# Kernel optimization log

Measured on AMD Instinct MI355X. Metric: run time of the kernel, lower is better.

The kernel has to match this reference:

```python
import jax, jax.numpy as jnp
import numpy as np

N = 50000      # nodes
E = 800000     # edges (before self loops)
F_IN = 128     # num_features
H = 4          # heads
C = 32         # hidden_channels (per-head out dim)
L = 64         # num_labels


def gatv2_conv(x, src, dst, Wl, Wr, att, b, n):
    """PyG GATv2Conv (concat=True, negative_slope=0.2), self loops already in src/dst."""
    h, c = att.shape
    xl = (x @ Wl).reshape(n, h, c)          # source-side transform
    xr = (x @ Wr).reshape(n, h, c)          # target-side transform
    z = jax.nn.leaky_relu(xl[src] + xr[dst], 0.2)   # [Etot, H, C]
    e = jnp.einsum('ehc,hc->eh', z, att)            # attention logits per edge/head
    m = jax.ops.segment_max(e, dst, num_segments=n)  # per-destination softmax (stable)
    p = jnp.exp(e - m[dst])
    s = jax.ops.segment_sum(p, dst, num_segments=n)
    alpha = p / s[dst]                               # [Etot, H]
    out = jax.ops.segment_sum(xl[src] * alpha[..., None], dst, num_segments=n)
    return out.reshape(n, h * c) + b


def setup_inputs() -> dict:
    key = jax.random.key(0)
    ks = jax.random.split(key, 16)
    sc = 0.1
    return {
        'x': jax.random.normal(ks[0], (N, F_IN), dtype=jnp.float32),
        'edge_index': jax.random.randint(ks[1], (2, E), 0, N),
        # conv1: F_IN -> H*C
        'Wl1': jax.random.normal(ks[2], (F_IN, H * C), dtype=jnp.float32) * sc,
        'Wr1': jax.random.normal(ks[3], (F_IN, H * C), dtype=jnp.float32) * sc,
        'att1': jax.random.normal(ks[4], (H, C), dtype=jnp.float32) * sc,
        'b1': jnp.zeros((H * C,), dtype=jnp.float32),
        # conv2: H*C -> H*C
        'Wl2': jax.random.normal(ks[5], (H * C, H * C), dtype=jnp.float32) * sc,
        'Wr2': jax.random.normal(ks[6], (H * C, H * C), dtype=jnp.float32) * sc,
        'att2': jax.random.normal(ks[7], (H, C), dtype=jnp.float32) * sc,
        'b2': jnp.zeros((H * C,), dtype=jnp.float32),
        # MLP head
        'W1': jax.random.normal(ks[8], (H * C, L * 10), dtype=jnp.float32) * sc,
        'bb1': jnp.zeros((L * 10,), dtype=jnp.float32),
        'W2': jax.random.normal(ks[9], (L * 10, L * 5), dtype=jnp.float32) * sc,
        'bb2': jnp.zeros((L * 5,), dtype=jnp.float32),
        'W3': jax.random.normal(ks[10], (L * 5, L), dtype=jnp.float32) * sc,
        'bb3': jnp.zeros((L,), dtype=jnp.float32),
    }


def reference(x, edge_index, Wl1, Wr1, att1, b1, Wl2, Wr2, att2, b2,
              W1, bb1, W2, bb2, W3, bb3):
    loops = jnp.arange(N, dtype=edge_index.dtype)
    src = jnp.concatenate([edge_index[0], loops])
    dst = jnp.concatenate([edge_index[1], loops])
    h = jax.nn.elu(gatv2_conv(x, src, dst, Wl1, Wr1, att1, b1, N))
    h = jax.nn.elu(gatv2_conv(h, src, dst, Wl2, Wr2, att2, b2, N))
    h = jax.nn.elu(h @ W1 + bb1)
    h = jax.nn.elu(h @ W2 + bb2)
    return jax.nn.sigmoid(h @ W3 + bb3)
```

## Files before the change

### kernel.cpp

```cpp
#include <hip/hip_runtime.h>
#include <cstdint>
#include <cstddef>

typedef _Float16 f16;
typedef __attribute__((ext_vector_type(2))) _Float16 f16x2;
typedef __attribute__((ext_vector_type(4))) _Float16 f16x4;
typedef __attribute__((ext_vector_type(8))) _Float16 f16x8;
typedef __attribute__((ext_vector_type(4))) float f32x4;
typedef unsigned int u32;
typedef unsigned short u16;

#define ROWCAP 48
#define BCAP   5120
#define ECH    4096

__device__ __forceinline__ float fast_elu(float v)
{
    return v > 0.f ? v : __expf(v) - 1.f;
}
__device__ __forceinline__ float fast_sigmoid(float v)
{
    return 1.f / (1.f + __expf(-v));
}

__device__ __forceinline__ void gload16(const f16* g, f16* l)
{
    __builtin_amdgcn_global_load_lds(
        (const __attribute__((address_space(1))) u32*)g,
        (__attribute__((address_space(3))) u32*)l, 16, 0, 0);
}

#define BM 128
#define BN 64
#define BK 64

__global__ __launch_bounds__(256)
void gemm_mfma(const f16* __restrict__ A, const f16* __restrict__ Bt,
               const float* __restrict__ bias,
               float* __restrict__ Cf, f16* __restrict__ Cp,
               int M, int N, int K, int act)
{
    __shared__ __align__(16) f16 sA[BM * BK];
    __shared__ __align__(16) f16 sB[BN * BK];
    const int t = threadIdx.x;
    const int w = t >> 6, lane = t & 63;
    const int lr = lane & 15, lg = lane >> 4;

    const int nwg = gridDim.x * gridDim.y;
    int orig = blockIdx.y * gridDim.x + blockIdx.x;
    int q = nwg >> 3, r = nwg & 7;
    int xcd = orig & 7, slotid = orig >> 3;
    int wgid = (xcd < r ? xcd * (q + 1) : r * (q + 1) + (xcd - r) * q) + slotid;
    int bx = wgid % gridDim.x;
    int by = wgid / gridDim.x;

    const int row0 = by * BM, col0 = bx * BN;
    const int wr = (w & 1) * 64, wc = (w >> 1) * 32;
    const int srow = lane >> 3, slot = lane & 7;

    f32x4 acc[4][2];
    #pragma unroll
    for (int m = 0; m < 4; ++m)
        #pragma unroll
        for (int n = 0; n < 2; ++n) acc[m][n] = (f32x4)0.f;

    for (int k0 = 0; k0 < K; k0 += BK) {
        #pragma unroll
        for (int i = 0; i < 4; ++i) {
            int ci = w * 4 + i;
            int row = ci * 8 + srow;
            const f16* g = A + (size_t)(row0 + row) * K + k0 + ((slot ^ (row & 7)) << 3);
            gload16(g, &sA[ci * 512]);
        }
        #pragma unroll
        for (int i = 0; i < 2; ++i) {
            int ci = w * 2 + i;
            int col = ci * 8 + srow;
            const f16* g = Bt + (size_t)(col0 + col) * K + k0 + ((slot ^ (col & 7)) << 3);
            gload16(g, &sB[ci * 512]);
        }
        __syncthreads();
        #pragma unroll
        for (int kk = 0; kk < 2; ++kk) {
            f16x8 af[4], bfr[2];
            #pragma unroll
            for (int m = 0; m < 4; ++m) {
                int row = wr + m * 16 + lr;
                af[m] = *(const f16x8*)&sA[row * 64 + (((kk * 4 + lg) ^ (lr & 7)) << 3)];
            }
            #pragma unroll
            for (int n = 0; n < 2; ++n) {
                int col = wc + n * 16 + lr;
                bfr[n] = *(const f16x8*)&sB[col * 64 + (((kk * 4 + lg) ^ (lr & 7)) << 3)];
            }
            #pragma unroll
            for (int m = 0; m < 4; ++m)
                #pragma unroll
                for (int n = 0; n < 2; ++n)
                    acc[m][n] = __builtin_amdgcn_mfma_f32_16x16x32_f16(af[m], bfr[n], acc[m][n], 0, 0, 0);
        }
        __syncthreads();
    }

    #pragma unroll
    for (int m = 0; m < 4; ++m) {
        int grow = row0 + wr + m * 16 + lg * 4;
        #pragma unroll
        for (int n = 0; n < 2; ++n) {
            int gcol = col0 + wc + n * 16 + lr;
            if (gcol >= N) continue;
            float bv = bias ? bias[gcol] : 0.f;
            #pragma unroll
            for (int q2 = 0; q2 < 4; ++q2) {
                int rr = grow + q2;
                if (rr >= M) continue;
                float v = acc[m][n][q2] + bv;
                if (act == 1)      v = fast_elu(v);
                else if (act == 2) v = fast_sigmoid(v);
                size_t o = (size_t)rr * N + gcol;
                if (Cf) Cf[o] = v;
                else Cp[o] = (f16)v;
            }
        }
    }
}

__global__ __launch_bounds__(256)
void gemm_mfma_f32a(const float* __restrict__ A32, const f16* __restrict__ Bt,
                    f16* __restrict__ Cp, int M, int N, int K)
{
    __shared__ __align__(16) f16 sA[BM * BK];
    __shared__ __align__(16) f16 sB[BN * BK];
    const int t = threadIdx.x;
    const int w = t >> 6, lane = t & 63;
    const int lr = lane & 15, lg = lane >> 4;

    const int nwg = gridDim.x * gridDim.y;
    int orig = blockIdx.y * gridDim.x + blockIdx.x;
    int q = nwg >> 3, r = nwg & 7;
    int xcd = orig & 7, slotid = orig >> 3;
    int wgid = (xcd < r ? xcd * (q + 1) : r * (q + 1) + (xcd - r) * q) + slotid;
    int bx = wgid % gridDim.x;
    int by = wgid / gridDim.x;

    const int row0 = by * BM, col0 = bx * BN;
    const int wr = (w & 1) * 64, wc = (w >> 1) * 32;
    const int srow = lane >> 3, slot = lane & 7;

    f32x4 acc[4][2];
    #pragma unroll
    for (int m = 0; m < 4; ++m)
        #pragma unroll
        for (int n = 0; n < 2; ++n) acc[m][n] = (f32x4)0.f;

    for (int k0 = 0; k0 < K; k0 += BK) {
        #pragma unroll
        for (int i = 0; i < 4; ++i) {
            int ci = w * 4 + i;
            int row = ci * 8 + srow;
            int grow = row0 + row;
            const float* g = A32 + (size_t)grow * K + k0 + ((slot ^ (row & 7)) << 3);
            float4 v0 = make_float4(0.f, 0.f, 0.f, 0.f), v1 = v0;
            if (grow < M) {
                v0 = *(const float4*)g;
                v1 = *(const float4*)(g + 4);
            }
            f16x8 h;
            h[0] = (f16)v0.x; h[1] = (f16)v0.y; h[2] = (f16)v0.z; h[3] = (f16)v0.w;
            h[4] = (f16)v1.x; h[5] = (f16)v1.y; h[6] = (f16)v1.z; h[7] = (f16)v1.w;
            *(f16x8*)&sA[ci * 512 + (lane << 3)] = h;
        }
        #pragma unroll
        for (int i = 0; i < 2; ++i) {
            int ci = w * 2 + i;
            int col = ci * 8 + srow;
            const f16* g = Bt + (size_t)(col0 + col) * K + k0 + ((slot ^ (col & 7)) << 3);
            gload16(g, &sB[ci * 512]);
        }
        __syncthreads();
        #pragma unroll
        for (int kk = 0; kk < 2; ++kk) {
            f16x8 af[4], bfr[2];
            #pragma unroll
            for (int m = 0; m < 4; ++m) {
                int row = wr + m * 16 + lr;
                af[m] = *(const f16x8*)&sA[row * 64 + (((kk * 4 + lg) ^ (lr & 7)) << 3)];
            }
            #pragma unroll
            for (int n = 0; n < 2; ++n) {
                int col = wc + n * 16 + lr;
                bfr[n] = *(const f16x8*)&sB[col * 64 + (((kk * 4 + lg) ^ (lr & 7)) << 3)];
            }
            #pragma unroll
            for (int m = 0; m < 4; ++m)
                #pragma unroll
                for (int n = 0; n < 2; ++n)
                    acc[m][n] = __builtin_amdgcn_mfma_f32_16x16x32_f16(af[m], bfr[n], acc[m][n], 0, 0, 0);
        }
        __syncthreads();
    }

    #pragma unroll
    for (int m = 0; m < 4; ++m) {
        int grow = row0 + wr + m * 16 + lg * 4;
        #pragma unroll
        for (int n = 0; n < 2; ++n) {
            int gcol = col0 + wc + n * 16 + lr;
            if (gcol >= N) continue;
            #pragma unroll
            for (int q2 = 0; q2 < 4; ++q2) {
                int rr = grow + q2;
                if (rr >= M) continue;
                Cp[(size_t)rr * N + gcol] = (f16)acc[m][n][q2];
            }
        }
    }
}

__global__ __launch_bounds__(256)
void prep_kernel(const float* __restrict__ Wl1, const float* __restrict__ Wr1,
                 const float* __restrict__ Wl2, const float* __restrict__ Wr2,
                 f16* __restrict__ T1c, f16* __restrict__ T2c,
                 const float* __restrict__ W1, const float* __restrict__ W2,
                 const float* __restrict__ W3,
                 f16* __restrict__ T1, f16* __restrict__ T2, f16* __restrict__ T3,
                 const int* __restrict__ ei, int E, int Etot,
                 int* __restrict__ gcnt, u32* __restrict__ bucketbuf,
                 int nbwc, int nbwm)
{
    int b = blockIdx.x;
    int tid = threadIdx.x;
    if (b < nbwc) {
        int i = b * 256 + tid;
        int sel = i >> 15;
        int j = i & 32767;
        int r = j >> 7, k = j & 127, n = r & 127;
        const float* W = sel ? (r < 128 ? Wl2 : Wr2) : (r < 128 ? Wl1 : Wr1);
        f16* T = sel ? T2c : T1c;
        T[(size_t)r * 128 + k] = (f16)W[(size_t)k * 128 + n];
        return;
    }
    if (b < nbwc + nbwm) {
        int i = (b - nbwc) * 256 + tid;
        const int n1 = 640 * 128, n2 = 320 * 640, n3 = 64 * 320;
        if (i < n1) {
            int n = i >> 7, k = i & 127;
            T1[i] = (f16)W1[(size_t)k * 640 + n];
        } else if (i < n1 + n2) {
            int j = i - n1;
            int n = j / 640, k = j - n * 640;
            T2[j] = (f16)W2[(size_t)k * 320 + n];
        } else if (i < n1 + n2 + n3) {
            int j = i - n1 - n2;
            int n = j / 320, k = j - n * 320;
            T3[j] = (f16)W3[(size_t)k * 64 + n];
        }
        return;
    }
    __shared__ int hist[256];
    __shared__ int base[256];
    int bb = b - nbwc - nbwm;
    int e0 = bb * ECH;
    hist[tid] = 0;
    __syncthreads();

    u32 pk[ECH / 256];
    #pragma unroll
    for (int i = 0; i < ECH / 256; ++i) {
        int e = e0 + i * 256 + tid;
        u32 p = 0xFFFFFFFFu;
        if (e < Etot) {
            int src, dst;
            if (e < E) {
                src = __builtin_nontemporal_load(ei + e);
                dst = __builtin_nontemporal_load(ei + E + e);
            } else {
                src = dst = e - E;
            }
            p = ((u32)dst << 16) | (u32)src;
            atomicAdd(&hist[dst >> 8], 1);
        }
        pk[i] = p;
    }
    __syncthreads();
    int h = hist[tid];
    base[tid] = h ? atomicAdd(&gcnt[tid], h) : 0;
    __syncthreads();
    hist[tid] = 0;
    __syncthreads();
    #pragma unroll
    for (int i = 0; i < ECH / 256; ++i) {
        u32 p = pk[i];
        if (p != 0xFFFFFFFFu) {
            int bu = p >> 24;
            int pos = base[bu] + atomicAdd(&hist[bu], 1);
            if (pos < BCAP)
                bucketbuf[(size_t)bu * BCAP + pos] = p;
        }
    }
}

__global__ __launch_bounds__(256)
void bucket2_kernel(const int* __restrict__ gcnt, const u32* __restrict__ bucketbuf,
                    int* __restrict__ cnt, u16* __restrict__ csrcp, int N)
{
    __shared__ u16 rows[256 * ROWCAP];
    __shared__ int rc[256];
    const int bu = blockIdx.x;
    const int tid = threadIdx.x;
    rc[tid] = 0;
    __syncthreads();

    int total = gcnt[bu];
    if (total > BCAP) total = BCAP;
    const u32* bp = bucketbuf + (size_t)bu * BCAP;
    for (int i = tid; i < total; i += 256) {
        u32 p = bp[i];
        int nid = (p >> 16) & 255;
        int pos = atomicAdd(&rc[nid], 1);
        if (pos < ROWCAP) rows[nid * ROWCAP + pos] = (u16)(p & 0xFFFFu);
    }
    __syncthreads();

    const int node0 = bu * 256;
    u32* d = (u32*)(csrcp + (size_t)node0 * ROWCAP);
    const u32* s = (const u32*)rows;
    const int nwords = 256 * ROWCAP / 2;
    for (int j = tid; j < nwords; j += 256) d[j] = s[j];
    int node = node0 + tid;
    if (node < N) {
        int c = rc[tid];
        cnt[node] = c < ROWCAP ? c : ROWCAP;
    }
}

__device__ __forceinline__ float dot2acc(f16x2 a, f16x2 b, float c)
{
#if __has_builtin(__builtin_amdgcn_fdot2)
    return __builtin_amdgcn_fdot2(a, b, c, false);
#else
    return c + (float)a.x * (float)b.x + (float)a.y * (float)b.y;
#endif
}

__device__ __forceinline__ f16x2 lrelu2(f16x2 v, f16x2 c02)
{
    return __builtin_elementwise_max(v, v * c02);
}

__global__ __launch_bounds__(256)
void gat_fused(const f16* __restrict__ xlxr,
               const int* __restrict__ cnt, const u16* __restrict__ csrcp,
               const float* __restrict__ att, const float* __restrict__ bias,
               f16* __restrict__ outp, int N)
{
    const int tid  = threadIdx.x;
    const int wave = tid >> 6;
    const int lane = tid & 63;
    const int half = lane >> 5;
    const int hl   = lane & 31;
    const int node = blockIdx.x * 8 + wave * 2 + half;
    const int c    = hl * 4;

    const bool valid = node < N;
    const int nd = valid ? node : 0;

    f16x2 alo; alo.x = (f16)att[c];     alo.y = (f16)att[c + 1];
    f16x2 ahi; ahi.x = (f16)att[c + 2]; ahi.y = (f16)att[c + 3];
    f16x2 c02; c02.x = (f16)0.2f;       c02.y = (f16)0.2f;
    f16x4 xr4 = *(const f16x4*)(xlxr + (size_t)nd * 256 + 128 + c);
    f16x2 xrlo = __builtin_shufflevector(xr4, xr4, 0, 1);
    f16x2 xrhi = __builtin_shufflevector(xr4, xr4, 2, 3);

    float acc0 = 0.f, acc1 = 0.f, acc2 = 0.f, acc3 = 0.f, s = 0.f;
    int e   = valid ? nd * ROWCAP : 0;
    int end = valid ? e + cnt[nd] : 0;

    for (; e + 4 <= end; e += 4) {
        int s0 = csrcp[e], s1 = csrcp[e + 1], s2 = csrcp[e + 2], s3 = csrcp[e + 3];
        f16x4 xa = *(const f16x4*)(xlxr + (size_t)s0 * 256 + c);
        f16x4 xb = *(const f16x4*)(xlxr + (size_t)s1 * 256 + c);
        f16x4 xc = *(const f16x4*)(xlxr + (size_t)s2 * 256 + c);
        f16x4 xd = *(const f16x4*)(xlxr + (size_t)s3 * 256 + c);
        f16x2 xalo = __builtin_shufflevector(xa, xa, 0, 1);
        f16x2 xahi = __builtin_shufflevector(xa, xa, 2, 3);
        f16x2 xblo = __builtin_shufflevector(xb, xb, 0, 1);
        f16x2 xbhi = __builtin_shufflevector(xb, xb, 2, 3);
        f16x2 xclo = __builtin_shufflevector(xc, xc, 0, 1);
        f16x2 xchi = __builtin_shufflevector(xc, xc, 2, 3);
        f16x2 xdlo = __builtin_shufflevector(xd, xd, 0, 1);
        f16x2 xdhi = __builtin_shufflevector(xd, xd, 2, 3);
        float za = dot2acc(lrelu2(xalo + xrlo, c02), alo,
                   dot2acc(lrelu2(xahi + xrhi, c02), ahi, 0.f));
        float zb = dot2acc(lrelu2(xblo + xrlo, c02), alo,
                   dot2acc(lrelu2(xbhi + xrhi, c02), ahi, 0.f));
        float zc = dot2acc(lrelu2(xclo + xrlo, c02), alo,
                   dot2acc(lrelu2(xchi + xrhi, c02), ahi, 0.f));
        float zd = dot2acc(lrelu2(xdlo + xrlo, c02), alo,
                   dot2acc(lrelu2(xdhi + xrhi, c02), ahi, 0.f));
        #pragma unroll
        for (int m = 1; m < 8; m <<= 1) {
            za += __shfl_xor(za, m, 64);
            zb += __shfl_xor(zb, m, 64);
            zc += __shfl_xor(zc, m, 64);
            zd += __shfl_xor(zd, m, 64);
        }
        float pa = __expf(za), pb = __expf(zb), pc = __expf(zc), pd = __expf(zd);
        s += (pa + pb) + (pc + pd);
        acc0 = fmaf(pa, (float)xa.x, fmaf(pb, (float)xb.x,
               fmaf(pc, (float)xc.x, fmaf(pd, (float)xd.x, acc0))));
        acc1 = fmaf(pa, (float)xa.y, fmaf(pb, (float)xb.y,
               fmaf(pc, (float)xc.y, fmaf(pd, (float)xd.y, acc1))));
        acc2 = fmaf(pa, (float)xa.z, fmaf(pb, (float)xb.z,
               fmaf(pc, (float)xc.z, fmaf(pd, (float)xd.z, acc2))));
        acc3 = fmaf(pa, (float)xa.w, fmaf(pb, (float)xb.w,
               fmaf(pc, (float)xc.w, fmaf(pd, (float)xd.w, acc3))));
    }
    for (; e < end; ++e) {
        int src = csrcp[e];
        f16x4 xv = *(const f16x4*)(xlxr + (size_t)src * 256 + c);
        f16x2 xlo = __builtin_shufflevector(xv, xv, 0, 1);
        f16x2 xhi = __builtin_shufflevector(xv, xv, 2, 3);
        float z = dot2acc(lrelu2(xlo + xrlo, c02), alo,
                  dot2acc(lrelu2(xhi + xrhi, c02), ahi, 0.f));
        #pragma unroll
        for (int m = 1; m < 8; m <<= 1)
            z += __shfl_xor(z, m, 64);
        float p = __expf(z);
        s += p;
        acc0 = fmaf(p, (float)xv.x, acc0);
        acc1 = fmaf(p, (float)xv.y, acc1);
        acc2 = fmaf(p, (float)xv.z, acc2);
        acc3 = fmaf(p, (float)xv.w, acc3);
    }

    if (valid) {
        float inv = 1.f / s;
        f16x4 o4;
        o4.x = (f16)fast_elu(acc0 * inv + bias[c]);
        o4.y = (f16)fast_elu(acc1 * inv + bias[c + 1]);
        o4.z = (f16)fast_elu(acc2 * inv + bias[c + 2]);
        o4.w = (f16)fast_elu(acc3 * inv + bias[c + 3]);
        *(f16x4*)(outp + (size_t)node * 128 + c) = o4;
    }
}

extern "C" void kernel_launch(void* const* d_in, const int* in_sizes, int n_in,
                              void* d_out, int out_size, void* d_ws, size_t ws_size,
                              hipStream_t stream)
{
    const float* x    = (const float*)d_in[0];
    const int*   ei   = (const int*)  d_in[1];
    const float* Wl1  = (const float*)d_in[2];
    const float* Wr1  = (const float*)d_in[3];
    const float* att1 = (const float*)d_in[4];
    const float* b1   = (const float*)d_in[5];
    const float* Wl2  = (const float*)d_in[6];
    const float* Wr2  = (const float*)d_in[7];
    const float* att2 = (const float*)d_in[8];
    const float* b2   = (const float*)d_in[9];
    const float* W1   = (const float*)d_in[10];
    const float* bb1  = (const float*)d_in[11];
    const float* W2   = (const float*)d_in[12];
    const float* bb2  = (const float*)d_in[13];
    const float* W3   = (const float*)d_in[14];
    const float* bb3  = (const float*)d_in[15];
    float* out = (float*)d_out;

    const int Nn   = in_sizes[0] / 128;
    const int E    = in_sizes[1] / 2;
    const int Etot = E + Nn;
    const int PAD  = 128;
    const int NBUCK = (Nn + 255) >> 8;

    char* base = (char*)d_ws;
    size_t woff = 0;
    auto alloc = [&](size_t bytes) -> void* {
        woff = (woff + 255) & ~(size_t)255;
        void* p = base + woff;
        woff += bytes;
        return p;
    };
    f16* xlxr  = (f16*)alloc((size_t)Nn * 256 * 2);
    f16* h1    = (f16*)alloc((size_t)(Nn + PAD) * 128 * 2);
    f16* h2    = (f16*)alloc((size_t)(Nn + PAD) * 128 * 2);
    f16* WLR1  = (f16*)alloc((size_t)256 * 128 * 2);
    f16* WLR2  = (f16*)alloc((size_t)256 * 128 * 2);
    f16* W1t   = (f16*)alloc((size_t)640 * 128 * 2);
    f16* W2t   = (f16*)alloc((size_t)320 * 640 * 2);
    f16* W3t   = (f16*)alloc((size_t)64 * 320 * 2);
    int* gcnt  = (int*)alloc((size_t)NBUCK * 4);
    int* cnt   = (int*)alloc((size_t)Nn * 4);
    u32* bucketbuf = (u32*)alloc((size_t)NBUCK * BCAP * 4);
    u16* csrcp = (u16*)alloc((size_t)NBUCK * 256 * ROWCAP * 2);

    dim3 blk(256);
    auto gemm = [&](const f16* A, const f16* Bt, const float* bias,
                    float* Cf, f16* Cp, int M, int N, int K, int act) {
        dim3 grid((N + BN - 1) / BN, (M + BM - 1) / BM);
        hipLaunchKernelGGL(gemm_mfma, grid, blk, 0, stream, A, Bt, bias, Cf, Cp, M, N, K, act);
    };

    const int eb   = (Etot + ECH - 1) / ECH;
    const int gatb = (Nn + 7) / 8;

    hipMemsetAsync(gcnt, 0, (size_t)NBUCK * sizeof(int), stream);
    const int nbwc = (2 * 256 * 128) / 256;
    const int nbwm = (640 * 128 + 320 * 640 + 64 * 320 + 255) / 256;
    hipLaunchKernelGGL(prep_kernel, dim3(nbwc + nbwm + eb), blk, 0, stream,
                       Wl1, Wr1, Wl2, Wr2, WLR1, WLR2,
                       W1, W2, W3, W1t, W2t, W3t,
                       ei, E, Etot, gcnt, bucketbuf, nbwc, nbwm);
    hipLaunchKernelGGL(bucket2_kernel, dim3(NBUCK), blk, 0, stream,
                       gcnt, bucketbuf, cnt, csrcp, Nn);

    {
        dim3 grid(256 / BN, (Nn + BM - 1) / BM);
        hipLaunchKernelGGL(gemm_mfma_f32a, grid, blk, 0, stream,
                           x, WLR1, xlxr, Nn, 256, 128);
    }
    hipLaunchKernelGGL(gat_fused, dim3(gatb), blk, 0, stream,
                       xlxr, cnt, csrcp, att1, b1, h1, Nn);

    gemm(h1, WLR2, nullptr, nullptr, xlxr, Nn, 256, 128, 0);
    hipLaunchKernelGGL(gat_fused, dim3(gatb), blk, 0, stream,
                       xlxr, cnt, csrcp, att2, b2, h2, Nn);

    size_t need = ((size_t)(Nn + PAD) * 640 + (size_t)(Nn + PAD) * 320) * 2 + 512;
    int CHUNK;
    f16 *t1, *t2;
    if (ws_size - woff >= need) {
        CHUNK = Nn;
        t1 = (f16*)alloc((size_t)(Nn + PAD) * 640 * 2);
        t2 = (f16*)alloc((size_t)(Nn + PAD) * 320 * 2);
    } else {
        CHUNK = 19000;
        t1 = (f16*)base;
        t2 = t1 + (size_t)(CHUNK + PAD) * 640;
    }
    for (int c0 = 0; c0 < Nn; c0 += CHUNK) {
        int cm = (Nn - c0) < CHUNK ? (Nn - c0) : CHUNK;
        gemm(h2 + (size_t)c0 * 128, W1t, bb1, nullptr, t1, cm, 640, 128, 1);
        gemm(t1, W2t, bb2, nullptr, t2, cm, 320, 640, 1);
        gemm(t2, W3t, bb3, out + (size_t)c0 * 64, nullptr, cm, 64, 320, 2);
    }
}
```

Measured before the change: 252.6 us.

## Fuse first two MLP GEMMs to keep the 640-wide hidden layer on-chip

Adds a kernel in which each 64-row block computes h2@W1 with ELU in 64-column slices and feeds each slice through lane shuffles straight into the W2 accumulation as MFMA A-fragments. The 640-wide intermediate activation is never written to or read back from global memory, and one launch is removed. In exchange, the W1 and W2 weights are read directly from global memory per wave with no shared-memory staging, each wave holds 20 accumulators (high register pressure), and the shuffle repacking adds work.

```diff
diff --git a/kernel.cpp b/kernel.cpp
--- a/kernel.cpp
+++ b/kernel.cpp
@@ -213,6 +213,87 @@
                 if (rr >= M) continue;
                 Cp[(size_t)rr * N + gcol] = (f16)acc[m][n][q2];
             }
+        }
+    }
+}
+
+__global__ __launch_bounds__(256)
+void mlp12_fused(const f16* __restrict__ h2, const f16* __restrict__ W1t,
+                 const f16* __restrict__ W2t, const float* __restrict__ bb1,
+                 const float* __restrict__ bb2, f16* __restrict__ t2, int M)
+{
+    __shared__ __align__(16) f16 sH[2][64 * 64];
+    const int t = threadIdx.x;
+    const int w = t >> 6, lane = t & 63;
+    const int lr = lane & 15, lg = lane >> 4;
+    const int row0 = blockIdx.x * 64;
+    const int srow = lane >> 3, slot = lane & 7;
+
+    #pragma unroll
+    for (int kt2 = 0; kt2 < 2; ++kt2) {
+        #pragma unroll
+        for (int i = 0; i < 2; ++i) {
+            int ci = w * 2 + i;
+            int row = ci * 8 + srow;
+            const f16* g = h2 + (size_t)(row0 + row) * 128 + kt2 * 64 + ((slot ^ (row & 7)) << 3);
+            gload16(g, &sH[kt2][ci * 512]);
+        }
+    }
+    __syncthreads();
+
+    f32x4 acc2[20];
+    #pragma unroll
+    for (int n = 0; n < 20; ++n) acc2[n] = (f32x4)0.f;
+
+    for (int kt = 0; kt < 10; ++kt) {
+        f32x4 a1[4];
+        #pragma unroll
+        for (int hf = 0; hf < 4; ++hf) a1[hf] = (f32x4)0.f;
+        #pragma unroll
+        for (int kk = 0; kk < 4; ++kk) {
+            int hrow = w * 16 + lr;
+            f16x8 hb = *(const f16x8*)&sH[kk >> 1][hrow * 64 + ((((kk & 1) * 4 + lg) ^ (lr & 7)) << 3)];
+            #pragma unroll
+            for (int hf = 0; hf < 4; ++hf) {
+                const f16* wp = W1t + (size_t)(kt * 64 + hf * 16 + lr) * 128 + kk * 32 + lg * 8;
+                f16x8 wa = *(const f16x8*)wp;
+                a1[hf] = __builtin_amdgcn_mfma_f32_16x16x32_f16(wa, hb, a1[hf], 0, 0, 0);
+            }
+        }
+        float tv[4][4];
+        #pragma unroll
+        for (int hf = 0; hf < 4; ++hf)
+            #pragma unroll
+            for (int qq = 0; qq < 4; ++qq)
+                tv[hf][qq] = fast_elu(a1[hf][qq] + bb1[kt * 64 + hf * 16 + lg * 4 + qq]);
+        #pragma unroll
+        for (int kk2 = 0; kk2 < 2; ++kk2) {
+            f16x8 af;
+            #pragma unroll
+            for (int j = 0; j < 8; ++j) {
+                int srcLane = (2 * (lg & 1) + (j >> 2)) * 16 + lr;
+                float v0 = __shfl(tv[kk2 * 2 + 0][j & 3], srcLane, 64);
+                float v1 = __shfl(tv[kk2 * 2 + 1][j & 3], srcLane, 64);
+                af[j] = (f16)((lg >> 1) ? v1 : v0);
+            }
+            #pragma unroll
+            for (int nf = 0; nf < 20; ++nf) {
+                const f16* wp = W2t + (size_t)(nf * 16 + lr) * 640 + kt * 64 + kk2 * 32 + lg * 8;
+                f16x8 bf = *(const f16x8*)wp;
+                acc2[nf] = __builtin_amdgcn_mfma_f32_16x16x32_f16(af, bf, acc2[nf], 0, 0, 0);
+            }
+        }
+    }
+
+    #pragma unroll
+    for (int nf = 0; nf < 20; ++nf) {
+        int col = nf * 16 + lr;
+        float bv = bb2[col];
+        #pragma unroll
+        for (int qq = 0; qq < 4; ++qq) {
+            int row = row0 + w * 16 + lg * 4 + qq;
+            if (row < M)
+                t2[(size_t)row * 320 + col] = (f16)fast_elu(acc2[nf][qq] + bv);
         }
     }
 }
@@ -493,6 +574,7 @@
     int* cnt   = (int*)alloc((size_t)Nn * 4);
     u32* bucketbuf = (u32*)alloc((size_t)NBUCK * BCAP * 4);
     u16* csrcp = (u16*)alloc((size_t)NBUCK * 256 * ROWCAP * 2);
+    f16* t2buf = (f16*)alloc((size_t)(Nn + PAD) * 320 * 2);
 
     dim3 blk(256);
     auto gemm = [&](const f16* A, const f16* Bt, const float* bias,
@@ -526,22 +608,7 @@
     hipLaunchKernelGGL(gat_fused, dim3(gatb), blk, 0, stream,
                        xlxr, cnt, csrcp, att2, b2, h2, Nn);
 
-    size_t need = ((size_t)(Nn + PAD) * 640 + (size_t)(Nn + PAD) * 320) * 2 + 512;
-    int CHUNK;
-    f16 *t1, *t2;
-    if (ws_size - woff >= need) {
-        CHUNK = Nn;
-        t1 = (f16*)alloc((size_t)(Nn + PAD) * 640 * 2);
-        t2 = (f16*)alloc((size_t)(Nn + PAD) * 320 * 2);
-    } else {
-        CHUNK = 19000;
-        t1 = (f16*)base;
-        t2 = t1 + (size_t)(CHUNK + PAD) * 640;
-    }
-    for (int c0 = 0; c0 < Nn; c0 += CHUNK) {
-        int cm = (Nn - c0) < CHUNK ? (Nn - c0) : CHUNK;
-        gemm(h2 + (size_t)c0 * 128, W1t, bb1, nullptr, t1, cm, 640, 128, 1);
-        gemm(t1, W2t, bb2, nullptr, t2, cm, 320, 640, 1);
-        gemm(t2, W3t, bb3, out + (size_t)c0 * 64, nullptr, cm, 64, 320, 2);
-    }
-}
+    hipLaunchKernelGGL(mlp12_fused, dim3((Nn + 63) / 64), blk, 0, stream,
+                       h2, W1t, W2t, bb1, bb2, t2buf, Nn);
+    gemm(t2buf, W3t, bb3, out, nullptr, Nn, 64, 320, 2);
+}
```

Result: slower. 459.3 us (+81.8%).
